# Kernel tuning notes

Hardware: AMD Instinct MI355X
Metric: run time of the kernel (lower is better)

Reference implementation:

```python
import jax, jax.numpy as jnp
import numpy as np

N, E = 50000, 800000
NODE_IN, EDGE_IN, HID, OUT = 64, 16, 64, 32
BN_EPS = 1e-5


def _linear_params(key, fan_in, fan_out):
    kw, kb = jax.random.split(key)
    lim = 1.0 / np.sqrt(fan_in)
    W = jax.random.uniform(kw, (fan_in, fan_out), minval=-lim, maxval=lim, dtype=jnp.float32)
    b = jax.random.uniform(kb, (fan_out,), minval=-lim, maxval=lim, dtype=jnp.float32)
    return W, b


def setup_inputs() -> dict:
    key = jax.random.key(0)
    ks = jax.random.split(key, 8)
    x = jax.random.normal(ks[0], (N, NODE_IN), dtype=jnp.float32)
    edge_index = jax.random.randint(ks[1], (2, E), 0, N, dtype=jnp.int64)
    edge_attr = jax.random.normal(ks[2], (E, EDGE_IN), dtype=jnp.float32)
    # layer 1: message Linear(node_in + edge_in -> hid), self Linear(node_in -> hid)
    W1_msg, b1_msg = _linear_params(ks[3], NODE_IN + EDGE_IN, HID)
    W1_self, b1_self = _linear_params(ks[4], NODE_IN, HID)
    # BatchNorm1d(hidden) params (inference mode: running stats)
    bn_gamma = jnp.ones((HID,), jnp.float32)
    bn_beta = jnp.zeros((HID,), jnp.float32)
    bn_mean = jax.random.normal(ks[5], (HID,), dtype=jnp.float32) * 0.1
    bn_var = jax.random.uniform(ks[6], (HID,), minval=0.5, maxval=1.5, dtype=jnp.float32)
    # layer 2: message Linear(hid + edge_in -> out), self Linear(hid -> out)
    k7, k8 = jax.random.split(ks[7])
    W2_msg, b2_msg = _linear_params(k7, HID + EDGE_IN, OUT)
    W2_self, b2_self = _linear_params(k8, HID, OUT)
    return dict(x=x, edge_index=edge_index, edge_attr=edge_attr,
                W1_msg=W1_msg, b1_msg=b1_msg, W1_self=W1_self, b1_self=b1_self,
                bn_gamma=bn_gamma, bn_beta=bn_beta, bn_mean=bn_mean, bn_var=bn_var,
                W2_msg=W2_msg, b2_msg=b2_msg, W2_self=W2_self, b2_self=b2_self)


def _gnn_layer(x, edge_index, edge_attr, W_msg, b_msg, W_self, b_self):
    # gather source node features per edge, concat edge features, linear, scatter-sum to dst
    src, dst = edge_index[0], edge_index[1]
    m = jnp.concatenate([x[src], edge_attr], axis=-1) @ W_msg + b_msg  # [E, out]
    agg = jax.ops.segment_sum(m, dst, num_segments=x.shape[0])          # [N, out]
    return x @ W_self + b_self + agg


def reference(x, edge_index, edge_attr,
              W1_msg, b1_msg, W1_self, b1_self,
              bn_gamma, bn_beta, bn_mean, bn_var,
              W2_msg, b2_msg, W2_self, b2_self):
    h = _gnn_layer(x, edge_index, edge_attr, W1_msg, b1_msg, W1_self, b1_self)
    # BatchNorm1d (eval mode, running stats) + ReLU; dropout is identity in eval
    h = (h - bn_mean) * jax.lax.rsqrt(bn_var + BN_EPS) * bn_gamma + bn_beta
    h = jax.nn.relu(h)
    return _gnn_layer(h, edge_index, edge_attr, W2_msg, b2_msg, W2_self, b2_self)
```

## Files before the change

### kernel.cpp

```cpp
#include <hip/hip_runtime.h>

#define NN 50000
#define NE 800000
#define NB 6250
#define NT 3125
#define NBK 128
#define BNODE 391
#define BCAP 7680
#define SCAP 56

typedef __attribute__((ext_vector_type(8))) short short8x;
typedef __attribute__((ext_vector_type(4))) float f32x4;

#define OFF_CNT   0LL
#define OFF_ROW   ((long long)NN)
#define OFF_RECS  (3LL*NN + 16)
#define OFF_FLAGS (35LL*NN + 16)
#define OFF_BS    (35LL*NN + 32)
#define OFF_BO    (35LL*NN + 96)
#define OFF_PK    (35LL*NN + 256)
#define OFF_FB1S  (35LL*NN + 7936)
#define OFF_FB2S  (35LL*NN + 8000)
#define OFF_F1    (36LL*NN)
#define OFF_F2    (116LL*NN)
#define OFF_Y2B   (164LL*NN)
#define OFF_S2    (180LL*NN)
#define OFF_BCUR  (212LL*NN)

__device__ __forceinline__ float ldf(const void* p, long long i, int bf16) {
  if (bf16) {
    unsigned short u = ((const unsigned short*)p)[i];
    return __uint_as_float(((unsigned)u) << 16);
  }
  return ((const float*)p)[i];
}
__device__ __forceinline__ unsigned short f2bf(float f) {
  unsigned u = __float_as_uint(f);
  unsigned r = (u + 0x7fffu + ((u >> 16) & 1u)) >> 16;
  return (unsigned short)r;
}
__device__ __forceinline__ unsigned pk2(float lo, float hi) {
  return (unsigned)f2bf(lo) | ((unsigned)f2bf(hi) << 16);
}
__device__ __forceinline__ int ldidx(const void* p, long long i, int i64) {
  return i64 ? (int)((const long long*)p)[i] : ((const int*)p)[i];
}
__device__ __forceinline__ float bflo(unsigned u) { return __uint_as_float(u << 16); }
__device__ __forceinline__ float bfhi(unsigned u) { return __uint_as_float(u & 0xffff0000u); }

__global__ void k_detect(const void* ei, const void* x, int* flags) {
  int lane = threadIdx.x & 63;
  const int* p = (const int*)ei;
  int any = 0;
  for (int i = lane; i < 256; i += 64) any |= p[2 * i + 1];
  unsigned long long anyb = __ballot(any != 0);
  const unsigned short* q = (const unsigned short*)x;
  int cnt = 0;
  for (int i = lane; i < 256; i += 64) {
    unsigned short w = q[2 * i];
    int e = (w >> 7) & 0xff;
    if (w == 0 || (e >= 110 && e <= 140)) cnt++;
  }
  for (int m = 1; m < 64; m <<= 1) cnt += __shfl_xor(cnt, m, 64);
  if (lane == 0) {
    flags[0] = (anyb == 0ull) ? 1 : 0;
    flags[1] = (cnt >= 192) ? 1 : 0;
  }
}

__global__ __launch_bounds__(256) void k_prep(
    const void* __restrict__ W1_msg, const void* __restrict__ b1_msg,
    const void* __restrict__ W1_self, const void* __restrict__ b1_self,
    const void* __restrict__ gamma, const void* __restrict__ beta,
    const void* __restrict__ mean, const void* __restrict__ var,
    const void* __restrict__ W2_msg, const void* __restrict__ b2_msg,
    const void* __restrict__ W2_self, const void* __restrict__ b2_self,
    const int* __restrict__ flags, unsigned short* __restrict__ PK,
    float* __restrict__ fb1s, float* __restrict__ fb2s) {
  int bf = flags[1];
  int t0 = blockIdx.x * 256 + threadIdx.x;
  int stride = gridDim.x * 256;
  for (int i = t0; i < 10240; i += stride) {
    int j = i & 7, L = (i >> 3) & 63, t = (i >> 9) & 3, c = i >> 11;
    int k = c * 32 + ((L >> 4) << 3) + j;
    int col = t * 16 + (L & 15);
    float sc = ldf(gamma, col, bf) * rsqrtf(ldf(var, col, bf) + 1e-5f);
    float v;
    if (k < 64) v = ldf(W1_msg, k * 64 + col, bf) * sc;
    else if (k < 128) v = ldf(W1_self, (k - 64) * 64 + col, bf) * sc;
    else if (k < 144) v = ldf(W1_msg, (64 + k - 128) * 64 + col, bf) * sc;
    else if (k == 144) v = ldf(b1_msg, col, bf) * sc;
    else v = 0.0f;
    PK[i] = f2bf(v);
  }
  for (int i = t0; i < 2048; i += stride) {
    int j = i & 7, L = (i >> 3) & 63, t = (i >> 9) & 1, c = i >> 10;
    int k = c * 32 + ((L >> 4) << 3) + j;
    int col = t * 16 + (L & 15);
    PK[10240 + i] = f2bf(ldf(W2_msg, k * 32 + col, bf));
  }
  for (int i = t0; i < 3072; i += stride) {
    int j = i & 7, L = (i >> 3) & 63, t = (i >> 9) & 1, c = i >> 10;
    int k = c * 32 + ((L >> 4) << 3) + j;
    int col = t * 16 + (L & 15);
    float v;
    if (k < 64) v = ldf(W2_self, k * 32 + col, bf);
    else if (k < 80) v = ldf(W2_msg, k * 32 + col, bf);
    else if (k == 80) v = ldf(b2_msg, col, bf);
    else v = 0.0f;
    PK[12288 + i] = f2bf(v);
  }
  for (int i = t0; i < 64; i += stride) {
    float sc = ldf(gamma, i, bf) * rsqrtf(ldf(var, i, bf) + 1e-5f);
    fb1s[i] = ldf(b1_self, i, bf) * sc + ldf(beta, i, bf) - ldf(mean, i, bf) * sc;
  }
  for (int i = t0; i < 32; i += stride) fb2s[i] = ldf(b2_self, i, bf);
}

__global__ __launch_bounds__(256) void k_bin(const void* __restrict__ ei,
                                             const int* __restrict__ flags,
                                             int* __restrict__ bcur,
                                             int2* __restrict__ binbuf) {
  __shared__ int2 stage[NBK][SCAP];
  __shared__ int scnt[NBK];
  __shared__ int gbase[NBK];
  int tid = threadIdx.x;
  for (int i = tid; i < NBK; i += 256) scnt[i] = 0;
  __syncthreads();
  int i64 = flags[0];
  for (long long e0 = (long long)blockIdx.x * 256; e0 < NE;
       e0 += (long long)gridDim.x * 256) {
    long long e = e0 + tid;
    if (e < NE) {
      int src = ldidx(ei, e, i64);
      int dst = ldidx(ei, NE + e, i64);
      int b = dst / BNODE;
      int dl = dst - b * BNODE;
      int2 ent = make_int2(src | (dl << 16), (int)e);
      int pos = atomicAdd(&scnt[b], 1);
      if (pos < SCAP) {
        stage[b][pos] = ent;
      } else {
        int gp = atomicAdd(&bcur[b], 1);
        binbuf[(long long)b * BCAP + gp] = ent;
      }
    }
  }
  __syncthreads();
  if (tid < NBK) {
    int cb = scnt[tid] < SCAP ? scnt[tid] : SCAP;
    gbase[tid] = atomicAdd(&bcur[tid], cb);
  }
  __syncthreads();
  for (int b = 0; b < NBK; ++b) {
    int cb = scnt[b] < SCAP ? scnt[b] : SCAP;
    for (int i = tid; i < cb; i += 256)
      binbuf[(long long)b * BCAP + gbase[b] + i] = stage[b][i];
  }
}

__global__ void k_scan128(const int* __restrict__ bcur, int* __restrict__ bo) {
  __shared__ int s[NBK];
  int t = threadIdx.x;
  int orig = bcur[t];
  s[t] = orig;
  __syncthreads();
  for (int off = 1; off < NBK; off <<= 1) {
    int u = (t >= off) ? s[t - off] : 0;
    __syncthreads();
    s[t] += u;
    __syncthreads();
  }
  bo[t] = s[t] - orig;
}

__global__ __launch_bounds__(256) void k_place(const int* __restrict__ bcur,
                                               const int2* __restrict__ binbuf,
                                               const int* __restrict__ bo,
                                               int* __restrict__ row_ptr,
                                               int2* __restrict__ recs) {
  __shared__ int2 outb[BCAP];
  __shared__ int lh[BNODE];
  __shared__ int lexc[BNODE];
  __shared__ int lcur[BNODE];
  int b = blockIdx.x;
  int tid = threadIdx.x;
  int base = b * BNODE;
  int nn = NN - base < BNODE ? NN - base : BNODE;
  int cnt = bcur[b];
  int rbase = bo[b];
  for (int i = tid; i < BNODE; i += 256) lh[i] = 0;
  __syncthreads();
  for (int i = tid; i < cnt; i += 256) {
    int dl = (binbuf[(long long)b * BCAP + i].x >> 16) & 0x3FF;
    atomicAdd(&lh[dl], 1);
  }
  __syncthreads();
  if (tid < 64) {
    int carry = 0;
    for (int c0 = 0; c0 < BNODE; c0 += 64) {
      int i = c0 + tid;
      int orig = (i < nn) ? lh[i] : 0;
      int v = orig;
      for (int off = 1; off < 64; off <<= 1) {
        int u = __shfl_up(v, off, 64);
        if (tid >= off) v += u;
      }
      if (i < nn) lexc[i] = carry + v - orig;
      carry += __shfl(v, 63, 64);
    }
  }
  __syncthreads();
  for (int i = tid; i < nn; i += 256) {
    int e = lexc[i];
    row_ptr[base + i] = rbase + e;
    lcur[i] = e;
  }
  if (b == NBK - 1 && tid == 0) row_ptr[NN] = rbase + cnt;
  __syncthreads();
  for (int i = tid; i < cnt; i += 256) {
    int2 ent = binbuf[(long long)b * BCAP + i];
    int dl = (ent.x >> 16) & 0x3FF;
    int p = atomicAdd(&lcur[dl], 1);
    outb[p] = make_int2(ent.x & 0xFFFF, ent.y);
  }
  __syncthreads();
  for (int i = tid; i < cnt; i += 256) recs[rbase + i] = outb[i];
}

__global__ __launch_bounds__(256) void k_gather1(
    const void* __restrict__ x, const void* __restrict__ ea,
    const int* __restrict__ row_ptr, const int2* __restrict__ recs,
    const int* __restrict__ flags, unsigned short* __restrict__ F1,
    unsigned short* __restrict__ F2) {
  int lane = threadIdx.x & 63;
  int g = lane >> 3, c = lane & 7;
  int bf = flags[1];
  long long wid = ((long long)blockIdx.x * blockDim.x + threadIdx.x) >> 6;
  long long nw = ((long long)gridDim.x * blockDim.x) >> 6;
  for (long long b = wid; b < NB; b += nw) {
    int n = (int)(b * 8 + g);
    int beg = row_ptr[n];
    int deg = row_ptr[n + 1] - beg;
    float a0 = 0.f, a1 = 0.f, a2 = 0.f, a3 = 0.f, a4 = 0.f, a5 = 0.f, a6 = 0.f, a7 = 0.f;
    float e0 = 0.f, e1 = 0.f, e2 = 0.f, e3 = 0.f;
    uint4 xw;
    if (bf) {
      const unsigned short* xs = (const unsigned short*)x;
      const unsigned short* es = (const unsigned short*)ea;
      int t = 0;
      for (; t + 4 <= deg; t += 4) {
        int2 r0 = recs[beg + t + 0];
        int2 r1 = recs[beg + t + 1];
        int2 r2 = recs[beg + t + 2];
        int2 r3 = recs[beg + t + 3];
        uint4 w0 = *((const uint4*)(xs + ((long long)r0.x << 6)) + c);
        uint4 w1 = *((const uint4*)(xs + ((long long)r1.x << 6)) + c);
        uint4 w2 = *((const uint4*)(xs + ((long long)r2.x << 6)) + c);
        uint4 w3 = *((const uint4*)(xs + ((long long)r3.x << 6)) + c);
        a0 += bflo(w0.x) + bflo(w1.x) + bflo(w2.x) + bflo(w3.x);
        a1 += bfhi(w0.x) + bfhi(w1.x) + bfhi(w2.x) + bfhi(w3.x);
        a2 += bflo(w0.y) + bflo(w1.y) + bflo(w2.y) + bflo(w3.y);
        a3 += bfhi(w0.y) + bfhi(w1.y) + bfhi(w2.y) + bfhi(w3.y);
        a4 += bflo(w0.z) + bflo(w1.z) + bflo(w2.z) + bflo(w3.z);
        a5 += bfhi(w0.z) + bfhi(w1.z) + bfhi(w2.z) + bfhi(w3.z);
        a6 += bflo(w0.w) + bflo(w1.w) + bflo(w2.w) + bflo(w3.w);
        a7 += bfhi(w0.w) + bfhi(w1.w) + bfhi(w2.w) + bfhi(w3.w);
        if (c < 4) {
          uint2 q0 = *((const uint2*)(es + ((long long)r0.y << 4)) + c);
          uint2 q1 = *((const uint2*)(es + ((long long)r1.y << 4)) + c);
          uint2 q2 = *((const uint2*)(es + ((long long)r2.y << 4)) + c);
          uint2 q3 = *((const uint2*)(es + ((long long)r3.y << 4)) + c);
          e0 += bflo(q0.x) + bflo(q1.x) + bflo(q2.x) + bflo(q3.x);
          e1 += bfhi(q0.x) + bfhi(q1.x) + bfhi(q2.x) + bfhi(q3.x);
          e2 += bflo(q0.y) + bflo(q1.y) + bflo(q2.y) + bflo(q3.y);
          e3 += bfhi(q0.y) + bfhi(q1.y) + bfhi(q2.y) + bfhi(q3.y);
        }
      }
      for (; t < deg; ++t) {
        int2 r = recs[beg + t];
        uint4 w = *((const uint4*)(xs + ((long long)r.x << 6)) + c);
        a0 += bflo(w.x); a1 += bfhi(w.x);
        a2 += bflo(w.y); a3 += bfhi(w.y);
        a4 += bflo(w.z); a5 += bfhi(w.z);
        a6 += bflo(w.w); a7 += bfhi(w.w);
        if (c < 4) {
          uint2 q = *((const uint2*)(es + ((long long)r.y << 4)) + c);
          e0 += bflo(q.x); e1 += bfhi(q.x);
          e2 += bflo(q.y); e3 += bfhi(q.y);
        }
      }
      xw = *((const uint4*)(xs + ((long long)n << 6)) + c);
    } else {
      const float* xf = (const float*)x;
      const float* ef = (const float*)ea;
      for (int t = 0; t < deg; ++t) {
        int2 r = recs[beg + t];
        float4 w0 = *((const float4*)(xf + ((long long)r.x << 6)) + c * 2);
        float4 w1 = *((const float4*)(xf + ((long long)r.x << 6)) + c * 2 + 1);
        a0 += w0.x; a1 += w0.y; a2 += w0.z; a3 += w0.w;
        a4 += w1.x; a5 += w1.y; a6 += w1.z; a7 += w1.w;
        if (c < 4) {
          float4 q = *((const float4*)(ef + ((long long)r.y << 4)) + c);
          e0 += q.x; e1 += q.y; e2 += q.z; e3 += q.w;
        }
      }
      float4 p0 = *((const float4*)(xf + ((long long)n << 6)) + c * 2);
      float4 p1 = *((const float4*)(xf + ((long long)n << 6)) + c * 2 + 1);
      xw = make_uint4(pk2(p0.x, p0.y), pk2(p0.z, p0.w), pk2(p1.x, p1.y), pk2(p1.z, p1.w));
    }
    unsigned short* f1 = F1 + (long long)n * 160;
    unsigned short* f2 = F2 + (long long)n * 96;
    *((uint4*)f1 + c) = make_uint4(pk2(a0, a1), pk2(a2, a3), pk2(a4, a5), pk2(a6, a7));
    *((uint4*)(f1 + 64) + c) = xw;
    if (c < 4) {
      uint2 sp = make_uint2(pk2(e0, e1), pk2(e2, e3));
      *((uint2*)(f1 + 128) + c) = sp;
      *((uint2*)(f2 + 64) + c) = sp;
    }
    if (c == 4) {
      unsigned d = (unsigned)f2bf((float)deg);
      *((uint4*)(f1 + 144)) = make_uint4(d, 0u, 0u, 0u);
      *((uint4*)(f2 + 80)) = make_uint4(d, 0u, 0u, 0u);
    }
    if (c == 5) {
      *((uint4*)(f1 + 152)) = make_uint4(0u, 0u, 0u, 0u);
      *((uint4*)(f2 + 88)) = make_uint4(0u, 0u, 0u, 0u);
    }
  }
}

__global__ __launch_bounds__(256) void k_gemm1(
    const unsigned short* __restrict__ F1, const unsigned short* __restrict__ PK,
    const float* __restrict__ fb1s, unsigned short* __restrict__ F2,
    unsigned short* __restrict__ Y2B) {
  __shared__ unsigned short hsh[4][16 * 72];
  int lane = threadIdx.x & 63;
  int wv = threadIdx.x >> 6;
  int m = lane & 15, quad = lane >> 4;
  unsigned short* hs = hsh[wv];
  short8x Bf[20];
#pragma unroll
  for (int s = 0; s < 20; ++s) Bf[s] = *(const short8x*)(PK + (s * 64 + lane) * 8);
  short8x By[4];
#pragma unroll
  for (int s = 0; s < 4; ++s) By[s] = *(const short8x*)(PK + 10240 + (s * 64 + lane) * 8);
  long long gw = (long long)blockIdx.x * 4 + wv;
  long long nw = (long long)gridDim.x * 4;
  for (long long tile = gw; tile < NT; tile += nw) {
    long long n0 = tile * 16;
    const unsigned short* f1 = F1 + (n0 + m) * 160 + quad * 8;
    short8x A[5];
#pragma unroll
    for (int cc = 0; cc < 5; ++cc) A[cc] = *(const short8x*)(f1 + cc * 32);
    f32x4 acc[4];
#pragma unroll
    for (int t = 0; t < 4; ++t) {
      float b = fb1s[t * 16 + m];
      acc[t] = (f32x4){b, b, b, b};
    }
#pragma unroll
    for (int cc = 0; cc < 5; ++cc) {
#pragma unroll
      for (int t = 0; t < 4; ++t)
        acc[t] = __builtin_amdgcn_mfma_f32_16x16x32_bf16(A[cc], Bf[cc * 4 + t], acc[t], 0, 0, 0);
    }
#pragma unroll
    for (int t = 0; t < 4; ++t) {
#pragma unroll
      for (int i = 0; i < 4; ++i) {
        float h = fmaxf(acc[t][i], 0.0f);
        unsigned short us = f2bf(h);
        F2[(n0 + quad * 4 + i) * 96 + t * 16 + m] = us;
        hs[(quad * 4 + i) * 72 + t * 16 + m] = us;
      }
    }
    __builtin_amdgcn_sched_barrier(0);
    f32x4 yacc[2];
    yacc[0] = (f32x4){0.f, 0.f, 0.f, 0.f};
    yacc[1] = (f32x4){0.f, 0.f, 0.f, 0.f};
#pragma unroll
    for (int cc = 0; cc < 2; ++cc) {
      short8x Ah = *(const short8x*)(hs + m * 72 + cc * 32 + quad * 8);
#pragma unroll
      for (int t = 0; t < 2; ++t)
        yacc[t] = __builtin_amdgcn_mfma_f32_16x16x32_bf16(Ah, By[cc * 2 + t], yacc[t], 0, 0, 0);
    }
#pragma unroll
    for (int t = 0; t < 2; ++t) {
#pragma unroll
      for (int i = 0; i < 4; ++i)
        Y2B[(n0 + quad * 4 + i) * 32 + t * 16 + m] = f2bf(yacc[t][i]);
    }
    __builtin_amdgcn_sched_barrier(0);
  }
}

__global__ __launch_bounds__(256) void k_gather2(
    const unsigned short* __restrict__ Y2B, const int* __restrict__ row_ptr,
    const int2* __restrict__ recs, float* __restrict__ S2) {
  int lane = threadIdx.x & 63;
  int g = lane >> 3, c = lane & 7;
  long long wid = ((long long)blockIdx.x * blockDim.x + threadIdx.x) >> 6;
  long long nw = ((long long)gridDim.x * blockDim.x) >> 6;
  for (long long b = wid; b < NB; b += nw) {
    int n = (int)(b * 8 + g);
    int beg = row_ptr[n];
    int deg = row_ptr[n + 1] - beg;
    float s0 = 0.f, s1 = 0.f, s2 = 0.f, s3 = 0.f;
    int t = 0;
    for (; t + 4 <= deg; t += 4) {
      int2 r0 = recs[beg + t + 0];
      int2 r1 = recs[beg + t + 1];
      int2 r2 = recs[beg + t + 2];
      int2 r3 = recs[beg + t + 3];
      uint2 q0 = *((const uint2*)(Y2B + (long long)r0.x * 32) + c);
      uint2 q1 = *((const uint2*)(Y2B + (long long)r1.x * 32) + c);
      uint2 q2 = *((const uint2*)(Y2B + (long long)r2.x * 32) + c);
      uint2 q3 = *((const uint2*)(Y2B + (long long)r3.x * 32) + c);
      s0 += bflo(q0.x) + bflo(q1.x) + bflo(q2.x) + bflo(q3.x);
      s1 += bfhi(q0.x) + bfhi(q1.x) + bfhi(q2.x) + bfhi(q3.x);
      s2 += bflo(q0.y) + bflo(q1.y) + bflo(q2.y) + bflo(q3.y);
      s3 += bfhi(q0.y) + bfhi(q1.y) + bfhi(q2.y) + bfhi(q3.y);
    }
    for (; t < deg; ++t) {
      int2 r = recs[beg + t];
      uint2 q = *((const uint2*)(Y2B + (long long)r.x * 32) + c);
      s0 += bflo(q.x); s1 += bfhi(q.x);
      s2 += bflo(q.y); s3 += bfhi(q.y);
    }
    *(float4*)(S2 + (long long)n * 32 + c * 4) = make_float4(s0, s1, s2, s3);
  }
}

__global__ __launch_bounds__(256) void k_gemm2(
    const unsigned short* __restrict__ F2, const unsigned short* __restrict__ PK,
    const float* __restrict__ fb2s, const float* __restrict__ S2,
    const int* __restrict__ flags, void* __restrict__ out) {
  int lane = threadIdx.x & 63;
  int wv = threadIdx.x >> 6;
  int m = lane & 15, quad = lane >> 4;
  int bf = flags[1];
  short8x Bf[6];
#pragma unroll
  for (int s = 0; s < 6; ++s) Bf[s] = *(const short8x*)(PK + 12288 + (s * 64 + lane) * 8);
  long long gw = (long long)blockIdx.x * 4 + wv;
  long long nw = (long long)gridDim.x * 4;
  for (long long tile = gw; tile < NT; tile += nw) {
    long long n0 = tile * 16;
    const unsigned short* f2 = F2 + (n0 + m) * 96 + quad * 8;
    short8x A[3];
#pragma unroll
    for (int cc = 0; cc < 3; ++cc) A[cc] = *(const short8x*)(f2 + cc * 32);
    f32x4 acc[2];
#pragma unroll
    for (int t = 0; t < 2; ++t) {
      float b = fb2s[t * 16 + m];
#pragma unroll
      for (int i = 0; i < 4; ++i)
        acc[t][i] = b + S2[(n0 + quad * 4 + i) * 32 + t * 16 + m];
    }
#pragma unroll
    for (int cc = 0; cc < 3; ++cc) {
#pragma unroll
      for (int t = 0; t < 2; ++t)
        acc[t] = __builtin_amdgcn_mfma_f32_16x16x32_bf16(A[cc], Bf[cc * 2 + t], acc[t], 0, 0, 0);
    }
#pragma unroll
    for (int t = 0; t < 2; ++t) {
#pragma unroll
      for (int i = 0; i < 4; ++i) {
        long long idx = (n0 + quad * 4 + i) * 32 + t * 16 + m;
        if (bf) ((unsigned short*)out)[idx] = f2bf(acc[t][i]);
        else ((float*)out)[idx] = acc[t][i];
      }
    }
  }
}

extern "C" void kernel_launch(void* const* d_in, const int* in_sizes, int n_in,
                              void* d_out, int out_size, void* d_ws, size_t ws_size,
                              hipStream_t stream) {
  const void* x = d_in[0];
  const void* ei = d_in[1];
  const void* ea = d_in[2];
  const void* W1_msg = d_in[3];
  const void* b1_msg = d_in[4];
  const void* W1_self = d_in[5];
  const void* b1_self = d_in[6];
  const void* gamma = d_in[7];
  const void* beta = d_in[8];
  const void* mean = d_in[9];
  const void* var = d_in[10];
  const void* W2_msg = d_in[11];
  const void* b2_msg = d_in[12];
  const void* W2_self = d_in[13];
  const void* b2_self = d_in[14];

  float* ws = (float*)d_ws;
  int* row_ptr = (int*)(ws + OFF_ROW);
  int2* recs = (int2*)(ws + OFF_RECS);
  int* flags = (int*)(ws + OFF_FLAGS);
  int* bo = (int*)(ws + OFF_BO);
  unsigned short* PK = (unsigned short*)(ws + OFF_PK);
  float* fb1s = ws + OFF_FB1S;
  float* fb2s = ws + OFF_FB2S;
  unsigned short* F1 = (unsigned short*)(ws + OFF_F1);
  int2* binbuf = (int2*)(ws + OFF_F1);
  unsigned short* F2 = (unsigned short*)(ws + OFF_F2);
  unsigned short* Y2B = (unsigned short*)(ws + OFF_Y2B);
  float* S2 = ws + OFF_S2;
  int* bcur = (int*)(ws + OFF_BCUR);

  hipLaunchKernelGGL(k_detect, dim3(1), dim3(64), 0, stream, ei, x, flags);
  hipMemsetAsync(bcur, 0, NBK * sizeof(int), stream);
  hipLaunchKernelGGL(k_prep, dim3(64), dim3(256), 0, stream, W1_msg, b1_msg, W1_self,
                     b1_self, gamma, beta, mean, var, W2_msg, b2_msg, W2_self, b2_self,
                     flags, PK, fb1s, fb2s);

  hipLaunchKernelGGL(k_bin, dim3(256), dim3(256), 0, stream, ei, flags, bcur, binbuf);
  hipLaunchKernelGGL(k_scan128, dim3(1), dim3(NBK), 0, stream, bcur, bo);
  hipLaunchKernelGGL(k_place, dim3(NBK), dim3(256), 0, stream, bcur, binbuf, bo,
                     row_ptr, recs);

  int gblocks = (NB + 3) / 4;
  hipLaunchKernelGGL(k_gather1, dim3(gblocks), dim3(256), 0, stream, x, ea, row_ptr,
                     recs, flags, F1, F2);
  int mblocks = (NT + 3) / 4;
  hipLaunchKernelGGL(k_gemm1, dim3(mblocks), dim3(256), 0, stream, F1, PK, fb1s, F2,
                     Y2B);
  hipLaunchKernelGGL(k_gather2, dim3(gblocks), dim3(256), 0, stream, Y2B, row_ptr, recs,
                     S2);
  hipLaunchKernelGGL(k_gemm2, dim3(mblocks), dim3(256), 0, stream, F2, PK, fb2s, S2,
                     flags, d_out);
}
```

Baseline: 241.4 us.

## Fold detect and scan kernels into neighbors and widen placement blocks

Merges the dtype/index detection into k_prep, where every block recomputes the bf16 flag locally, and removes the standalone 128-element scan kernel by having each k_place block compute its own prefix offset with a wavefront reduction. k_place now runs 1024 threads per block, and k_bin's stage flush gives each wave its own buckets instead of looping all bins with the whole block. The aim is to cut two kernel launches and their serialization gaps from the short preprocessing chain and to speed up the binning and placement steps. The risk is redundant flag detection in every prep block and lower occupancy for the larger k_place blocks, which also carry heavy shared-memory use.

```diff
diff --git a/kernel.cpp b/kernel.cpp
--- a/kernel.cpp
+++ b/kernel.cpp
@@ -16,7 +16,6 @@
 #define OFF_ROW   ((long long)NN)
 #define OFF_RECS  (3LL*NN + 16)
 #define OFF_FLAGS (35LL*NN + 16)
-#define OFF_BS    (35LL*NN + 32)
 #define OFF_BO    (35LL*NN + 96)
 #define OFF_PK    (35LL*NN + 256)
 #define OFF_FB1S  (35LL*NN + 7936)
@@ -48,37 +47,44 @@
 __device__ __forceinline__ float bflo(unsigned u) { return __uint_as_float(u << 16); }
 __device__ __forceinline__ float bfhi(unsigned u) { return __uint_as_float(u & 0xffff0000u); }
 
-__global__ void k_detect(const void* ei, const void* x, int* flags) {
-  int lane = threadIdx.x & 63;
-  const int* p = (const int*)ei;
-  int any = 0;
-  for (int i = lane; i < 256; i += 64) any |= p[2 * i + 1];
-  unsigned long long anyb = __ballot(any != 0);
-  const unsigned short* q = (const unsigned short*)x;
-  int cnt = 0;
-  for (int i = lane; i < 256; i += 64) {
-    unsigned short w = q[2 * i];
-    int e = (w >> 7) & 0xff;
-    if (w == 0 || (e >= 110 && e <= 140)) cnt++;
-  }
-  for (int m = 1; m < 64; m <<= 1) cnt += __shfl_xor(cnt, m, 64);
-  if (lane == 0) {
-    flags[0] = (anyb == 0ull) ? 1 : 0;
-    flags[1] = (cnt >= 192) ? 1 : 0;
-  }
-}
-
 __global__ __launch_bounds__(256) void k_prep(
+    const void* __restrict__ ei, const void* __restrict__ x,
     const void* __restrict__ W1_msg, const void* __restrict__ b1_msg,
     const void* __restrict__ W1_self, const void* __restrict__ b1_self,
     const void* __restrict__ gamma, const void* __restrict__ beta,
     const void* __restrict__ mean, const void* __restrict__ var,
     const void* __restrict__ W2_msg, const void* __restrict__ b2_msg,
     const void* __restrict__ W2_self, const void* __restrict__ b2_self,
-    const int* __restrict__ flags, unsigned short* __restrict__ PK,
+    int* __restrict__ flags, unsigned short* __restrict__ PK,
     float* __restrict__ fb1s, float* __restrict__ fb2s) {
-  int bf = flags[1];
-  int t0 = blockIdx.x * 256 + threadIdx.x;
+  __shared__ int s_bf;
+  int tid = threadIdx.x;
+  int lane = tid & 63;
+  if (tid < 64) {
+    const unsigned short* q = (const unsigned short*)x;
+    int cntc = 0;
+    for (int i = lane; i < 256; i += 64) {
+      unsigned short w = q[2 * i];
+      int e = (w >> 7) & 0xff;
+      if (w == 0 || (e >= 110 && e <= 140)) cntc++;
+    }
+    for (int m = 1; m < 64; m <<= 1) cntc += __shfl_xor(cntc, m, 64);
+    int bfv = (cntc >= 192) ? 1 : 0;
+    if (blockIdx.x == 0) {
+      const int* p = (const int*)ei;
+      int any = 0;
+      for (int i = lane; i < 256; i += 64) any |= p[2 * i + 1];
+      unsigned long long anyb = __ballot(any != 0);
+      if (lane == 0) {
+        flags[0] = (anyb == 0ull) ? 1 : 0;
+        flags[1] = bfv;
+      }
+    }
+    if (lane == 0) s_bf = bfv;
+  }
+  __syncthreads();
+  int bf = s_bf;
+  int t0 = blockIdx.x * 256 + tid;
   int stride = gridDim.x * 256;
   for (int i = t0; i < 10240; i += stride) {
     int j = i & 7, L = (i >> 3) & 63, t = (i >> 9) & 3, c = i >> 11;
@@ -152,46 +158,41 @@
     gbase[tid] = atomicAdd(&bcur[tid], cb);
   }
   __syncthreads();
-  for (int b = 0; b < NBK; ++b) {
+  int wv = tid >> 6, ln = tid & 63;
+  for (int b = wv; b < NBK; b += 4) {
     int cb = scnt[b] < SCAP ? scnt[b] : SCAP;
-    for (int i = tid; i < cb; i += 256)
-      binbuf[(long long)b * BCAP + gbase[b] + i] = stage[b][i];
-  }
-}
-
-__global__ void k_scan128(const int* __restrict__ bcur, int* __restrict__ bo) {
-  __shared__ int s[NBK];
-  int t = threadIdx.x;
-  int orig = bcur[t];
-  s[t] = orig;
-  __syncthreads();
-  for (int off = 1; off < NBK; off <<= 1) {
-    int u = (t >= off) ? s[t - off] : 0;
-    __syncthreads();
-    s[t] += u;
-    __syncthreads();
-  }
-  bo[t] = s[t] - orig;
-}
-
-__global__ __launch_bounds__(256) void k_place(const int* __restrict__ bcur,
-                                               const int2* __restrict__ binbuf,
-                                               const int* __restrict__ bo,
-                                               int* __restrict__ row_ptr,
-                                               int2* __restrict__ recs) {
+    int gb = gbase[b];
+    for (int i = ln; i < cb; i += 64)
+      binbuf[(long long)b * BCAP + gb + i] = stage[b][i];
+  }
+}
+
+__global__ __launch_bounds__(1024) void k_place(const int* __restrict__ bcur,
+                                                const int2* __restrict__ binbuf,
+                                                int* __restrict__ row_ptr,
+                                                int2* __restrict__ recs) {
   __shared__ int2 outb[BCAP];
   __shared__ int lh[BNODE];
   __shared__ int lexc[BNODE];
   __shared__ int lcur[BNODE];
+  __shared__ int sb[NBK];
+  __shared__ int s_rbase;
   int b = blockIdx.x;
   int tid = threadIdx.x;
   int base = b * BNODE;
   int nn = NN - base < BNODE ? NN - base : BNODE;
-  int cnt = bcur[b];
-  int rbase = bo[b];
-  for (int i = tid; i < BNODE; i += 256) lh[i] = 0;
-  __syncthreads();
-  for (int i = tid; i < cnt; i += 256) {
+  if (tid < NBK) sb[tid] = bcur[tid];
+  for (int i = tid; i < BNODE; i += 1024) lh[i] = 0;
+  __syncthreads();
+  if (tid < 64) {
+    int v = (tid < b ? sb[tid] : 0) + (tid + 64 < b ? sb[tid + 64] : 0);
+    for (int off = 32; off > 0; off >>= 1) v += __shfl_down(v, off, 64);
+    if (tid == 0) s_rbase = v;
+  }
+  int cnt = sb[b];
+  __syncthreads();
+  int rbase = s_rbase;
+  for (int i = tid; i < cnt; i += 1024) {
     int dl = (binbuf[(long long)b * BCAP + i].x >> 16) & 0x3FF;
     atomicAdd(&lh[dl], 1);
   }
@@ -211,21 +212,21 @@
     }
   }
   __syncthreads();
-  for (int i = tid; i < nn; i += 256) {
+  for (int i = tid; i < nn; i += 1024) {
     int e = lexc[i];
     row_ptr[base + i] = rbase + e;
     lcur[i] = e;
   }
   if (b == NBK - 1 && tid == 0) row_ptr[NN] = rbase + cnt;
   __syncthreads();
-  for (int i = tid; i < cnt; i += 256) {
+  for (int i = tid; i < cnt; i += 1024) {
     int2 ent = binbuf[(long long)b * BCAP + i];
     int dl = (ent.x >> 16) & 0x3FF;
     int p = atomicAdd(&lcur[dl], 1);
     outb[p] = make_int2(ent.x & 0xFFFF, ent.y);
   }
   __syncthreads();
-  for (int i = tid; i < cnt; i += 256) recs[rbase + i] = outb[i];
+  for (int i = tid; i < cnt; i += 1024) recs[rbase + i] = outb[i];
 }
 
 __global__ __launch_bounds__(256) void k_gather1(
@@ -501,7 +502,6 @@
   int* row_ptr = (int*)(ws + OFF_ROW);
   int2* recs = (int2*)(ws + OFF_RECS);
   int* flags = (int*)(ws + OFF_FLAGS);
-  int* bo = (int*)(ws + OFF_BO);
   unsigned short* PK = (unsigned short*)(ws + OFF_PK);
   float* fb1s = ws + OFF_FB1S;
   float* fb2s = ws + OFF_FB2S;
@@ -512,16 +512,13 @@
   float* S2 = ws + OFF_S2;
   int* bcur = (int*)(ws + OFF_BCUR);
 
-  hipLaunchKernelGGL(k_detect, dim3(1), dim3(64), 0, stream, ei, x, flags);
   hipMemsetAsync(bcur, 0, NBK * sizeof(int), stream);
-  hipLaunchKernelGGL(k_prep, dim3(64), dim3(256), 0, stream, W1_msg, b1_msg, W1_self,
-                     b1_self, gamma, beta, mean, var, W2_msg, b2_msg, W2_self, b2_self,
-                     flags, PK, fb1s, fb2s);
-
+  hipLaunchKernelGGL(k_prep, dim3(64), dim3(256), 0, stream, ei, x, W1_msg, b1_msg,
+                     W1_self, b1_self, gamma, beta, mean, var, W2_msg, b2_msg, W2_self,
+                     b2_self, flags, PK, fb1s, fb2s);
   hipLaunchKernelGGL(k_bin, dim3(256), dim3(256), 0, stream, ei, flags, bcur, binbuf);
-  hipLaunchKernelGGL(k_scan128, dim3(1), dim3(NBK), 0, stream, bcur, bo);
-  hipLaunchKernelGGL(k_place, dim3(NBK), dim3(256), 0, stream, bcur, binbuf, bo,
-                     row_ptr, recs);
+  hipLaunchKernelGGL(k_place, dim3(NBK), dim3(1024), 0, stream, bcur, binbuf, row_ptr,
+                     recs);
 
   int gblocks = (NB + 3) / 4;
   hipLaunchKernelGGL(k_gather1, dim3(gblocks), dim3(256), 0, stream, x, ea, row_ptr,
```

Measured after the change: 223.5 us. -7.4%, faster.
